# Optimization experiments

Hardware: AMD Instinct MI355X
Metric: run time of the kernel (lower is better)

The kernel has to match this reference:

```python
import jax, jax.numpy as jnp
import numpy as np

B, D, T, G = 8, 40, 192, 256
UNITS, DEMO, OUT = 256, 16, 1


def setup_inputs() -> dict:
    key = jax.random.key(0)
    ks = jax.random.split(key, 10)
    # observation timestamps, sorted, shared across channels (per preprocessing tile)
    t1 = jnp.sort(jax.random.uniform(ks[0], (B, T)) * 48.0, axis=-1)
    times = jnp.broadcast_to(t1[:, None, :], (B, D, T))
    values = jax.random.normal(ks[1], (B, D, T))
    meas = (jax.random.uniform(ks[2], (B, D, T)) < 0.5).astype(jnp.float32)
    meas = meas.at[:, :, 0].set(1.0)  # guarantee >=1 observation per channel
    grid = jnp.broadcast_to(jnp.linspace(0.0, 48.0, G)[None, :], (B, G))
    grid_lengths = jnp.concatenate([
        jax.random.randint(ks[3], (B - 1,), G // 2, G + 1, dtype=jnp.int32),
        jnp.array([G], dtype=jnp.int32)])
    demo = jax.random.normal(ks[4], (B, DEMO))
    # learned parameters
    kernel_sic = jnp.zeros((D,))                       # softplus-param RBF widths
    cross_W = jnp.eye(D)                               # identity init
    demo_W1 = jax.random.normal(ks[5], (DEMO, UNITS)) * 0.1
    demo_b1 = jnp.zeros((UNITS,))
    demo_W2 = jax.random.normal(ks[6], (UNITS, UNITS)) * 0.05
    demo_b2 = jnp.zeros((UNITS,))
    gru_Wx = jax.random.normal(ks[7], (3 * D, 3 * UNITS)) * 0.05
    gru_Wh = jax.random.normal(ks[8], (UNITS, 3 * UNITS)) * 0.05
    gru_b = jnp.zeros((2, 3 * UNITS))                  # keras reset_after=True: [input_bias, recurrent_bias]
    out_W = jax.random.normal(ks[9], (UNITS, OUT)) * 0.1
    out_b = jnp.zeros((OUT,))
    return dict(demo=demo, times=times, values=values, measurements=meas,
                grid=grid, kernel_sic=kernel_sic, cross_W=cross_W,
                demo_W1=demo_W1, demo_b1=demo_b1, demo_W2=demo_W2, demo_b2=demo_b2,
                gru_Wx=gru_Wx, gru_Wh=gru_Wh, gru_b=gru_b,
                out_W=out_W, out_b=out_b, grid_lengths=grid_lengths)


def _forward(demo, times, values, meas, grid, kernel_sic, cross_W,
             demo_W1, demo_b1, demo_W2, demo_b2,
             gru_Wx, gru_Wh, gru_b, out_W, out_b, grid_lengths):
    # ---- single_channel_interp (reconstruction=False) ----
    logmask = jnp.where(meas > 0, 0.0, -jnp.inf)[:, :, :, None]   # [B,D,T,1]
    norm = (times[:, :, :, None] - grid[:, None, None, :]) ** 2   # [B,D,T,G]
    alpha = jax.nn.softplus(kernel_sic)[None, :, None, None]      # [1,D,1,1]

    def interp(scale):
        logits = -scale * alpha * norm + logmask                  # [B,D,T,G]
        w = jax.nn.logsumexp(logits, axis=2)                      # [B,D,G]
        p = jnp.exp(logits - w[:, :, None, :])                    # softmax over T
        y = jnp.sum(p * values[:, :, :, None], axis=2)            # [B,D,G]
        return y, w

    y, w = interp(1.0)            # smooth interpolant + log-intensity
    y_trans, _ = interp(10.0)     # sharper (transient) interpolant

    # ---- cross_channel_interp (reconstruction=False) ----
    yT = jnp.swapaxes(y, 1, 2)                                    # [B,G,D]
    wT = jnp.swapaxes(w, 1, 2)
    sw = jax.nn.softmax(wT, axis=2)                               # softmax over channels
    mean = jnp.mean(yT, axis=1, keepdims=True)                    # [B,1,D]
    rep = jnp.einsum('bgd,de->bge', sw * (yT - mean), cross_W) + mean
    rep1 = jnp.swapaxes(rep, 1, 2)                                # [B,D,G]
    intensity = jnp.exp(w)
    feats = jnp.concatenate([rep1, intensity, y_trans - rep1], axis=1)  # [B,3D,G]
    rnn_in = jnp.swapaxes(feats, 1, 2)                            # [B,G,3D]

    # ---- demo encoder -> GRU initial state ----
    h0 = jax.nn.relu(demo @ demo_W1 + demo_b1) @ demo_W2 + demo_b2

    # ---- masked GRU (keras v2, reset_after=True), return last state ----
    bi, br = gru_b[0], gru_b[1]
    Gn = rnn_in.shape[1]
    seq_mask = jnp.arange(Gn)[None, :] < grid_lengths[:, None]    # [B,G]
    x_proj = rnn_in @ gru_Wx + bi                                 # [B,G,3U]

    def step(h, inp):
        xp, m = inp                                               # [B,3U], [B]
        hp = h @ gru_Wh + br
        xz, xr, xh = jnp.split(xp, 3, axis=-1)
        hz, hr, hh = jnp.split(hp, 3, axis=-1)
        z = jax.nn.sigmoid(xz + hz)
        r = jax.nn.sigmoid(xr + hr)
        cand = jnp.tanh(xh + r * hh)
        h_new = z * h + (1.0 - z) * cand
        return jnp.where(m[:, None], h_new, h), None

    h_final, _ = jax.lax.scan(step, h0,
                              (jnp.swapaxes(x_proj, 0, 1), seq_mask.T))
    return jax.nn.sigmoid(h_final @ out_W + out_b)                # [B,OUT]


def reference(demo, times, values, measurements, grid, kernel_sic, cross_W,
              demo_W1, demo_b1, demo_W2, demo_b2,
              gru_Wx, gru_Wh, gru_b, out_W, out_b, grid_lengths):
    return _forward(demo, times, values, measurements, grid, kernel_sic, cross_W,
                    demo_W1, demo_b1, demo_W2, demo_b2,
                    gru_Wx, gru_Wh, gru_b, out_W, out_b, grid_lengths)
```

## Files before the change

kernel.cpp:

```cpp
#include <hip/hip_runtime.h>
#include <hip/hip_bf16.h>

#define B_ 8
#define D_ 40
#define T_ 192
#define G_ 256
#define U_ 768
#define H_ 256

__device__ inline float sigmoidf_(float x){
  return 1.0f/(1.0f+__expf(-x));
}
__device__ inline float tanhf_(float x){
  float ax = fabsf(x);
  float e = __expf(-2.0f*ax);
  float t = (1.0f-e)/(1.0f+e);
  return copysignf(t, x);
}
__device__ inline int sdot4(int a, int b, int c){
#if __has_builtin(__builtin_amdgcn_sdot4)
  return __builtin_amdgcn_sdot4(a, b, c, false);
#else
  int r = c;
  #pragma unroll
  for (int i=0;i<4;i++){
    int ai = (a << (24-8*i)) >> 24;
    int bi = (b << (24-8*i)) >> 24;
    r += ai*bi;
  }
  return r;
#endif
}
__device__ inline int pack4(int q0,int q1,int q2,int q3){
  return (q0&255) | ((q1&255)<<8) | ((q2&255)<<16) | ((q3&255)<<24);
}

__global__ __launch_bounds__(256) void k_interp(
    const float* __restrict__ times, const float* __restrict__ values,
    const float* __restrict__ meas, const float* __restrict__ grid,
    const float* __restrict__ ksic,
    float* __restrict__ y, float* __restrict__ w, float* __restrict__ ytr,
    float* __restrict__ mean){
  int bd = blockIdx.x;
  int b = bd / D_, d = bd % D_;
  int g = threadIdx.x;
  __shared__ float tt[T_], vv[T_], mm[T_];
  __shared__ float red[256];
  if (g < T_){
    tt[g] = times[bd*T_+g];
    vv[g] = values[bd*T_+g];
    mm[g] = meas[bd*T_+g];
  }
  __syncthreads();
  float alpha = log1pf(__expf(ksic[d]));
  float tg = grid[b*G_+g];
  float nmin = 3.4e38f;
  for (int t=0;t<T_;t++){
    if (mm[t] > 0.0f){
      float dd = tt[t]-tg;
      nmin = fminf(nmin, dd*dd);
    }
  }
  float s1=0.f, sv1=0.f, s10=0.f, sv10=0.f;
  for (int t=0;t<T_;t++){
    if (mm[t] > 0.0f){
      float dd = tt[t]-tg;
      float n = dd*dd - nmin;
      float e1  = __expf(-alpha*n);
      float e10 = __expf(-10.0f*alpha*n);
      s1 += e1;  sv1 += e1*vv[t];
      s10 += e10; sv10 += e10*vv[t];
    }
  }
  float yv = sv1/s1;
  float wv = -alpha*nmin + __logf(s1);
  y[bd*G_+g]   = yv;
  w[bd*G_+g]   = wv;
  ytr[bd*G_+g] = sv10/s10;
  red[g] = yv;
  __syncthreads();
  for (int s=128;s>0;s>>=1){
    if (g<s) red[g]+=red[g+s];
    __syncthreads();
  }
  if (g==0) mean[bd] = red[0]*(1.0f/(float)G_);
}

__global__ __launch_bounds__(256) void k_cross(
    const float* __restrict__ y, const float* __restrict__ w,
    const float* __restrict__ ytr, const float* __restrict__ mean,
    const float* __restrict__ crossW, const float* __restrict__ Wx,
    const float* __restrict__ gru_b, const int* __restrict__ lens,
    float* __restrict__ xproj){
  int bg = blockIdx.x;
  int b = bg >> 8, g = bg & 255;
  if (g >= lens[b]) return;
  __shared__ float wd[D_], yd[D_], ytrd[D_], md[D_], cc[D_], feats[3*D_];
  __shared__ float wstat[2];
  int tid = threadIdx.x;
  if (tid < D_){
    int idx = (b*D_+tid)*G_+g;
    wd[tid]=w[idx]; yd[tid]=y[idx]; ytrd[tid]=ytr[idx]; md[tid]=mean[b*D_+tid];
  }
  __syncthreads();
  if (tid==0){
    float mx=-3.4e38f;
    for (int d2=0;d2<D_;d2++) mx = fmaxf(mx, wd[d2]);
    float s=0.f;
    for (int d2=0;d2<D_;d2++) s += __expf(wd[d2]-mx);
    wstat[0]=mx; wstat[1]=1.0f/s;
  }
  __syncthreads();
  if (tid<D_){
    float sw = __expf(wd[tid]-wstat[0])*wstat[1];
    cc[tid] = sw*(yd[tid]-md[tid]);
  }
  __syncthreads();
  if (tid<D_){
    float acc=0.f;
    for (int d2=0;d2<D_;d2++) acc += cc[d2]*crossW[d2*D_+tid];
    float rep = acc + md[tid];
    feats[tid]       = rep;
    feats[D_+tid]    = __expf(wd[tid]);
    feats[2*D_+tid]  = ytrd[tid]-rep;
  }
  __syncthreads();
  for (int jj=0;jj<3;jj++){
    int j = tid + jj*256;
    float acc = gru_b[j];
    #pragma unroll 4
    for (int i=0;i<3*D_;i++) acc += feats[i]*Wx[i*U_+j];
    xproj[(size_t)bg*U_ + j] = acc;
  }
}

__global__ __launch_bounds__(256) void k_demo(
    const float* __restrict__ demo, const float* __restrict__ W1,
    const float* __restrict__ b1, const float* __restrict__ W2,
    const float* __restrict__ b2, float* __restrict__ h0){
  __shared__ float dl[B_*16];
  __shared__ float hid[B_*H_];
  int u = threadIdx.x;
  if (u < B_*16) dl[u] = demo[u];
  __syncthreads();
  float acc[B_];
  #pragma unroll
  for (int b=0;b<B_;b++) acc[b]=b1[u];
  for (int i=0;i<16;i++){
    float w1 = W1[i*H_+u];
    #pragma unroll
    for (int b=0;b<B_;b++) acc[b] += dl[b*16+i]*w1;
  }
  #pragma unroll
  for (int b=0;b<B_;b++) hid[b*H_+u] = fmaxf(acc[b],0.f);
  __syncthreads();
  #pragma unroll
  for (int b=0;b<B_;b++) acc[b]=b2[u];
  for (int k=0;k<H_;k++){
    float w2 = W2[k*H_+u];
    #pragma unroll
    for (int b=0;b<B_;b++) acc[b] += hid[b*H_+k]*w2;
  }
  #pragma unroll
  for (int b=0;b<B_;b++) h0[b*H_+u]=acc[b];
}

__global__ __launch_bounds__(256) void k_quant(
    const float* __restrict__ Wh, int* __restrict__ wsq,
    float* __restrict__ wmaxs){
  int c0 = blockIdx.x*64;
  int rg = threadIdx.x >> 6;
  int cc = threadIdx.x & 63;
  int col = c0 + cc;
  float v[64];
  float mx = 0.f;
  #pragma unroll
  for (int r=0;r<64;r++){
    v[r] = Wh[(size_t)(rg*64+r)*U_ + col];
    mx = fmaxf(mx, fabsf(v[r]));
  }
  __shared__ float cm[4][64];
  cm[rg][cc] = mx;
  __syncthreads();
  float m = fmaxf(fmaxf(cm[0][cc],cm[1][cc]), fmaxf(cm[2][cc],cm[3][cc]));
  float iw = (m>0.f)? 127.0f/m : 0.f;
  if (rg==0) wmaxs[col] = m;
  #pragma unroll
  for (int k=0;k<16;k++){
    int q0=(int)rintf(v[4*k+0]*iw), q1=(int)rintf(v[4*k+1]*iw),
        q2=(int)rintf(v[4*k+2]*iw), q3=(int)rintf(v[4*k+3]*iw);
    wsq[(size_t)(rg*16+k)*U_ + col] = pack4(q0,q1,q2,q3);
  }
}

__global__ __launch_bounds__(256, 1)
void k_gru(
    const int* __restrict__ wsq, const float* __restrict__ wmaxs,
    const float* __restrict__ gru_b,
    const float* __restrict__ xproj, const float* __restrict__ h0,
    const int* __restrict__ lens, const float* __restrict__ outW,
    const float* __restrict__ outb, float* __restrict__ out){
  int b = blockIdx.x;
  int j = threadIdx.x;

  __shared__ __align__(16) int hq[2][64];
  __shared__ float red[H_];
  __shared__ float shs[2];

  float hj = h0[b*H_+j];
  red[j] = fabsf(hj);
  __syncthreads();
  for (int st=128; st>0; st>>=1){
    if (j < st) red[j] = fmaxf(red[j], red[j+st]);
    __syncthreads();
  }
  if (j==0){
    float bound = fmaxf(red[0], 1.0f);
    shs[0] = 127.0f/bound;
    shs[1] = bound/127.0f;
  }
  __syncthreads();
  float inv_sh = shs[0];
  float s_h    = shs[1];

  float cm0 = wmaxs[j], cm1 = wmaxs[H_+j], cm2 = wmaxs[2*H_+j];
  float fz = (cm0*(1.0f/127.0f))*s_h;
  float fr = (cm1*(1.0f/127.0f))*s_h;
  float fh = (cm2*(1.0f/127.0f))*s_h;
  float brz = gru_b[U_+j], brr = gru_b[U_+H_+j], brh = gru_b[U_+2*H_+j];

  int wqz[64], wqr[64], wqh[64];
  #pragma unroll
  for (int k=0;k<64;k++) wqz[k] = wsq[(size_t)k*U_ + j];
  #pragma unroll
  for (int k=0;k<64;k++) wqr[k] = wsq[(size_t)k*U_ + H_ + j];
  #pragma unroll
  for (int k=0;k<64;k++) wqh[k] = wsq[(size_t)k*U_ + 2*H_ + j];

  {
    float qf = fmaxf(-127.f, fminf(127.f, rintf(hj*inv_sh)));
    ((signed char*)hq[0])[j] = (signed char)(int)qf;
  }
  int len = lens[b];
  const float* xbase = xproj + (size_t)b*G_*U_;
  float xpz = xbase[j], xpr = xbase[H_+j], xph = xbase[2*H_+j];
  __syncthreads();

  for (int g=0; g<len; g++){
    float nxz=0.f, nxr=0.f, nxh=0.f;
    if (g+1 < len){
      const float* xn = xbase + (size_t)(g+1)*U_;
      nxz = xn[j]; nxr = xn[H_+j]; nxh = xn[2*H_+j];
    }
    const int4* hc = (const int4*)hq[g&1];
    int az=0, ar=0, ah=0;
    #pragma unroll
    for (int c=0;c<16;c++){
      int4 hv = hc[c];
      az=sdot4(hv.x,wqz[4*c+0],az); ar=sdot4(hv.x,wqr[4*c+0],ar); ah=sdot4(hv.x,wqh[4*c+0],ah);
      az=sdot4(hv.y,wqz[4*c+1],az); ar=sdot4(hv.y,wqr[4*c+1],ar); ah=sdot4(hv.y,wqh[4*c+1],ah);
      az=sdot4(hv.z,wqz[4*c+2],az); ar=sdot4(hv.z,wqr[4*c+2],ar); ah=sdot4(hv.z,wqh[4*c+2],ah);
      az=sdot4(hv.w,wqz[4*c+3],az); ar=sdot4(hv.w,wqr[4*c+3],ar); ah=sdot4(hv.w,wqh[4*c+3],ah);
    }
    float z    = sigmoidf_(xpz + brz + fz*(float)az);
    float r    = sigmoidf_(xpr + brr + fr*(float)ar);
    float cand = tanhf_(xph + r*(brh + fh*(float)ah));
    hj = z*hj + (1.0f-z)*cand;
    float qf = fmaxf(-127.f, fminf(127.f, rintf(hj*inv_sh)));
    ((signed char*)hq[(g+1)&1])[j] = (signed char)(int)qf;
    __syncthreads();
    xpz = nxz; xpr = nxr; xph = nxh;
  }

  red[j] = hj*outW[j];
  __syncthreads();
  for (int st=128;st>0;st>>=1){
    if (j<st) red[j]+=red[j+st];
    __syncthreads();
  }
  if (j==0) out[b] = sigmoidf_(red[0]+outb[0]);
}

extern "C" void kernel_launch(void* const* d_in, const int* in_sizes, int n_in,
                              void* d_out, int out_size, void* d_ws, size_t ws_size,
                              hipStream_t stream) {
  const float* demo   = (const float*)d_in[0];
  const float* times  = (const float*)d_in[1];
  const float* values = (const float*)d_in[2];
  const float* meas   = (const float*)d_in[3];
  const float* grid   = (const float*)d_in[4];
  const float* ksic   = (const float*)d_in[5];
  const float* crossW = (const float*)d_in[6];
  const float* dW1    = (const float*)d_in[7];
  const float* db1    = (const float*)d_in[8];
  const float* dW2    = (const float*)d_in[9];
  const float* db2    = (const float*)d_in[10];
  const float* gWx    = (const float*)d_in[11];
  const float* gWh    = (const float*)d_in[12];
  const float* gb     = (const float*)d_in[13];
  const float* outW   = (const float*)d_in[14];
  const float* outb   = (const float*)d_in[15];
  const int*   lens   = (const int*)d_in[16];
  float* out = (float*)d_out;

  float* ws   = (float*)d_ws;
  float* y    = ws;
  float* w    = y    + B_*D_*G_;
  float* ytr  = w    + B_*D_*G_;
  float* mean = ytr  + B_*D_*G_;
  float* h0   = mean + B_*D_;
  float* xprj = h0   + B_*H_;
  int*   wsq  = (int*)(xprj + (size_t)B_*G_*U_);
  float* wmx  = (float*)(wsq + 64*U_);

  k_interp<<<B_*D_, 256, 0, stream>>>(times, values, meas, grid, ksic, y, w, ytr, mean);
  k_quant <<<12,    256, 0, stream>>>(gWh, wsq, wmx);
  k_demo  <<<1,     256, 0, stream>>>(demo, dW1, db1, dW2, db2, h0);
  k_cross <<<B_*G_, 256, 0, stream>>>(y, w, ytr, mean, crossW, gWx, gb, lens, xprj);
  k_gru   <<<B_,    256, 0, stream>>>(wsq, wmx, gb, xprj, h0, lens, outW, outb, out);
}
```

Measured before the change: 305.5 us.

## Pair two batches per GRU block and split K-reduction across half-blocks

The GRU kernel now runs one 512-thread block per pair of batch rows. Each half-block holds half of the quantized recurrent weights in registers and computes partial dot products for both batches. Partials are exchanged through shared memory. The aim is to halve the per-step serial dot-product length and the register pressure per thread. In exchange it adds an extra barrier and an LDS exchange per step, and both batches step to the longer sequence length. The x-projection prefetch of the next step was also removed.

After: 396.4 us. +29.7%, slower.

```diff
diff --git a/kernel.cpp b/kernel.cpp
--- a/kernel.cpp
+++ b/kernel.cpp
@@ -193,35 +193,41 @@
   }
 }
 
-__global__ __launch_bounds__(256, 1)
+__global__ __launch_bounds__(512, 1)
 void k_gru(
     const int* __restrict__ wsq, const float* __restrict__ wmaxs,
     const float* __restrict__ gru_b,
     const float* __restrict__ xproj, const float* __restrict__ h0,
     const int* __restrict__ lens, const float* __restrict__ outW,
     const float* __restrict__ outb, float* __restrict__ out){
-  int b = blockIdx.x;
-  int j = threadIdx.x;
-
-  __shared__ __align__(16) int hq[2][64];
-  __shared__ float red[H_];
-  __shared__ float shs[2];
-
-  float hj = h0[b*H_+j];
-  red[j] = fabsf(hj);
+  int t = threadIdx.x;
+  int p = t >> 8;
+  int j = t & 255;
+  int bb = blockIdx.x*2 + p;
+
+  __shared__ __align__(16) int hq[2][2][64];
+  __shared__ int   ispart[3][512];
+  __shared__ float redf[2][256];
+  __shared__ float shs2[2][2];
+
+  float hj = h0[bb*H_+j];
+  redf[p][j] = fabsf(hj);
+  int lenA = lens[blockIdx.x*2], lenB = lens[blockIdx.x*2+1];
+  int len_max = max(lenA, lenB);
+  int mylen = p ? lenB : lenA;
   __syncthreads();
   for (int st=128; st>0; st>>=1){
-    if (j < st) red[j] = fmaxf(red[j], red[j+st]);
+    if (j < st) redf[p][j] = fmaxf(redf[p][j], redf[p][j+st]);
     __syncthreads();
   }
   if (j==0){
-    float bound = fmaxf(red[0], 1.0f);
-    shs[0] = 127.0f/bound;
-    shs[1] = bound/127.0f;
-  }
-  __syncthreads();
-  float inv_sh = shs[0];
-  float s_h    = shs[1];
+    float bound = fmaxf(redf[p][0], 1.0f);
+    shs2[p][0] = 127.0f/bound;
+    shs2[p][1] = bound/127.0f;
+  }
+  __syncthreads();
+  float inv_sh = shs2[p][0];
+  float s_h    = shs2[p][1];
 
   float cm0 = wmaxs[j], cm1 = wmaxs[H_+j], cm2 = wmaxs[2*H_+j];
   float fz = (cm0*(1.0f/127.0f))*s_h;
@@ -229,56 +235,73 @@
   float fh = (cm2*(1.0f/127.0f))*s_h;
   float brz = gru_b[U_+j], brr = gru_b[U_+H_+j], brh = gru_b[U_+2*H_+j];
 
-  int wqz[64], wqr[64], wqh[64];
-  #pragma unroll
-  for (int k=0;k<64;k++) wqz[k] = wsq[(size_t)k*U_ + j];
-  #pragma unroll
-  for (int k=0;k<64;k++) wqr[k] = wsq[(size_t)k*U_ + H_ + j];
-  #pragma unroll
-  for (int k=0;k<64;k++) wqh[k] = wsq[(size_t)k*U_ + 2*H_ + j];
-
+  int wqz[32], wqr[32], wqh[32];
+  #pragma unroll
+  for (int k=0;k<32;k++) wqz[k] = wsq[(size_t)(32*p+k)*U_ + j];
+  #pragma unroll
+  for (int k=0;k<32;k++) wqr[k] = wsq[(size_t)(32*p+k)*U_ + H_ + j];
+  #pragma unroll
+  for (int k=0;k<32;k++) wqh[k] = wsq[(size_t)(32*p+k)*U_ + 2*H_ + j];
+
+  int qb;
   {
     float qf = fmaxf(-127.f, fminf(127.f, rintf(hj*inv_sh)));
-    ((signed char*)hq[0])[j] = (signed char)(int)qf;
-  }
-  int len = lens[b];
-  const float* xbase = xproj + (size_t)b*G_*U_;
-  float xpz = xbase[j], xpr = xbase[H_+j], xph = xbase[2*H_+j];
-  __syncthreads();
-
-  for (int g=0; g<len; g++){
-    float nxz=0.f, nxr=0.f, nxh=0.f;
-    if (g+1 < len){
-      const float* xn = xbase + (size_t)(g+1)*U_;
-      nxz = xn[j]; nxr = xn[H_+j]; nxh = xn[2*H_+j];
-    }
-    const int4* hc = (const int4*)hq[g&1];
-    int az=0, ar=0, ah=0;
+    qb = (int)qf;
+    ((signed char*)hq[p][0])[j] = (signed char)qb;
+  }
+  const float* xbase = xproj + (size_t)bb*G_*U_;
+  __syncthreads();
+
+  for (int g=0; g<len_max; g++){
+    float xpz=0.f, xpr=0.f, xph=0.f;
+    if (g < mylen){
+      const float* xr = xbase + (size_t)g*U_;
+      xpz = xr[j]; xpr = xr[H_+j]; xph = xr[2*H_+j];
+    }
+    const int4* hA = ((const int4*)hq[0][g&1]) + p*8;
+    const int4* hB = ((const int4*)hq[1][g&1]) + p*8;
+    int az0=0,ar0=0,ah0=0, az1=0,ar1=0,ah1=0;
     #pragma unroll
-    for (int c=0;c<16;c++){
-      int4 hv = hc[c];
-      az=sdot4(hv.x,wqz[4*c+0],az); ar=sdot4(hv.x,wqr[4*c+0],ar); ah=sdot4(hv.x,wqh[4*c+0],ah);
-      az=sdot4(hv.y,wqz[4*c+1],az); ar=sdot4(hv.y,wqr[4*c+1],ar); ah=sdot4(hv.y,wqh[4*c+1],ah);
-      az=sdot4(hv.z,wqz[4*c+2],az); ar=sdot4(hv.z,wqr[4*c+2],ar); ah=sdot4(hv.z,wqh[4*c+2],ah);
-      az=sdot4(hv.w,wqz[4*c+3],az); ar=sdot4(hv.w,wqr[4*c+3],ar); ah=sdot4(hv.w,wqh[4*c+3],ah);
-    }
-    float z    = sigmoidf_(xpz + brz + fz*(float)az);
-    float r    = sigmoidf_(xpr + brr + fr*(float)ar);
-    float cand = tanhf_(xph + r*(brh + fh*(float)ah));
-    hj = z*hj + (1.0f-z)*cand;
-    float qf = fmaxf(-127.f, fminf(127.f, rintf(hj*inv_sh)));
-    ((signed char*)hq[(g+1)&1])[j] = (signed char)(int)qf;
-    __syncthreads();
-    xpz = nxz; xpr = nxr; xph = nxh;
-  }
-
-  red[j] = hj*outW[j];
+    for (int c=0;c<8;c++){
+      int4 u = hA[c];
+      az0=sdot4(u.x,wqz[4*c+0],az0); ar0=sdot4(u.x,wqr[4*c+0],ar0); ah0=sdot4(u.x,wqh[4*c+0],ah0);
+      az0=sdot4(u.y,wqz[4*c+1],az0); ar0=sdot4(u.y,wqr[4*c+1],ar0); ah0=sdot4(u.y,wqh[4*c+1],ah0);
+      az0=sdot4(u.z,wqz[4*c+2],az0); ar0=sdot4(u.z,wqr[4*c+2],ar0); ah0=sdot4(u.z,wqh[4*c+2],ah0);
+      az0=sdot4(u.w,wqz[4*c+3],az0); ar0=sdot4(u.w,wqr[4*c+3],ar0); ah0=sdot4(u.w,wqh[4*c+3],ah0);
+      int4 v = hB[c];
+      az1=sdot4(v.x,wqz[4*c+0],az1); ar1=sdot4(v.x,wqr[4*c+0],ar1); ah1=sdot4(v.x,wqh[4*c+0],ah1);
+      az1=sdot4(v.y,wqz[4*c+1],az1); ar1=sdot4(v.y,wqr[4*c+1],ar1); ah1=sdot4(v.y,wqh[4*c+1],ah1);
+      az1=sdot4(v.z,wqz[4*c+2],az1); ar1=sdot4(v.z,wqr[4*c+2],ar1); ah1=sdot4(v.z,wqh[4*c+2],ah1);
+      az1=sdot4(v.w,wqz[4*c+3],az1); ar1=sdot4(v.w,wqr[4*c+3],ar1); ah1=sdot4(v.w,wqh[4*c+3],ah1);
+      if (c==3) asm volatile("" ::: "memory");
+    }
+    ispart[0][t] = p ? az0 : az1;
+    ispart[1][t] = p ? ar0 : ar1;
+    ispart[2][t] = p ? ah0 : ah1;
+    __syncthreads();
+    int sz = (p ? az1 : az0) + ispart[0][t^256];
+    int sr = (p ? ar1 : ar0) + ispart[1][t^256];
+    int sh = (p ? ah1 : ah0) + ispart[2][t^256];
+    float z    = sigmoidf_(xpz + brz + fz*(float)sz);
+    float r    = sigmoidf_(xpr + brr + fr*(float)sr);
+    float cand = tanhf_(xph + r*(brh + fh*(float)sh));
+    float hn = z*hj + (1.0f-z)*cand;
+    if (g < mylen){
+      hj = hn;
+      float qf = fmaxf(-127.f, fminf(127.f, rintf(hj*inv_sh)));
+      qb = (int)qf;
+    }
+    ((signed char*)hq[p][(g+1)&1])[j] = (signed char)qb;
+    __syncthreads();
+  }
+
+  redf[p][j] = hj*outW[j];
   __syncthreads();
   for (int st=128;st>0;st>>=1){
-    if (j<st) red[j]+=red[j+st];
-    __syncthreads();
-  }
-  if (j==0) out[b] = sigmoidf_(red[0]+outb[0]);
+    if (j<st) redf[p][j] += redf[p][j+st];
+    __syncthreads();
+  }
+  if (j==0) out[bb] = sigmoidf_(redf[p][0]+outb[0]);
 }
 
 extern "C" void kernel_launch(void* const* d_in, const int* in_sizes, int n_in,
@@ -317,5 +340,5 @@
   k_quant <<<12,    256, 0, stream>>>(gWh, wsq, wmx);
   k_demo  <<<1,     256, 0, stream>>>(demo, dW1, db1, dW2, db2, h0);
   k_cross <<<B_*G_, 256, 0, stream>>>(y, w, ytr, mean, crossW, gWx, gb, lens, xprj);
-  k_gru   <<<B_,    256, 0, stream>>>(wsq, wmx, gb, xprj, h0, lens, outW, outb, out);
-}
+  k_gru   <<<B_/2,  512, 0, stream>>>(wsq, wmx, gb, xprj, h0, lens, outW, outb, out);
+}
```
